# Kernel tuning notes

Hardware: AMD Instinct MI355X
Metric: run time of the kernel (lower is better)

Reference implementation:

```python
import jax, jax.numpy as jnp
import numpy as np

NUM_TOKENS = 2048
HIDDEN = 1024
INTER = 2048
NUM_EXPERTS = 8
TOPK = 2


def setup_inputs() -> dict:
    key = jax.random.key(0)
    k1, k2, k3, k4 = jax.random.split(key, 4)
    hidden_states = jax.random.normal(k1, (NUM_TOKENS, HIDDEN), dtype=jnp.float32)
    router_logits = jax.random.normal(k2, (NUM_TOKENS, NUM_EXPERTS), dtype=jnp.float32)
    # fc1: [E, hidden, 2*intermediate] (proj/gate for SwiGLU), fc2: [E, intermediate, hidden]
    w1 = jax.random.normal(k3, (NUM_EXPERTS, HIDDEN, 2 * INTER), dtype=jnp.float32) * 0.02
    w2 = jax.random.normal(k4, (NUM_EXPERTS, INTER, HIDDEN), dtype=jnp.float32) * 0.02
    return {"hidden_states": hidden_states, "router_logits": router_logits, "w1": w1, "w2": w2}


def _grouped_gemm(x, w, expert_ids):
    """x: [T, D], w: [E, D, O], expert_ids: [T] -> [T, O].
    Tokens are routed to expert expert_ids[t]; equivalent to the sequential
    per-expert GEMM on contiguously sorted tokens. Small fixed loop over E."""
    out = jnp.zeros((x.shape[0], w.shape[-1]), dtype=x.dtype)
    for e in range(w.shape[0]):
        mask = (expert_ids == e)[:, None]
        out = out + jnp.where(mask, x, 0.0) @ w[e]
    return out


def reference(hidden_states, router_logits, w1, w2):
    # top-k routing + softmax over the selected logits
    top_logits, top_idx = jax.lax.top_k(router_logits, TOPK)      # [N, K]
    scores = jax.nn.softmax(top_logits, axis=-1)                  # [N, K]

    flat_idx = top_idx.reshape(-1)                                # [N*K]
    sorted_indices = jnp.argsort(flat_idx)                        # permute tokens grouped by expert
    permuted = hidden_states[sorted_indices // TOPK]              # [N*K, D]
    sorted_experts = flat_idx[sorted_indices]                     # [N*K] expert id per permuted row

    fc1_out = _grouped_gemm(permuted, w1, sorted_experts)         # [N*K, 2*I]
    proj, gate = jnp.split(fc1_out, 2, axis=-1)
    act = jax.nn.silu(proj) * gate                                # SwiGLU
    expert_out = _grouped_gemm(act, w2, sorted_experts)           # [N*K, D]

    # unpermute (scatter back) and weighted combine over top-k
    unpermuted = jnp.zeros_like(expert_out).at[sorted_indices].set(expert_out)
    unpermuted = unpermuted.reshape(-1, TOPK, expert_out.shape[-1])
    return (unpermuted * scores[..., None]).sum(axis=1)           # [N, D]
```

## Files before the change

### kernel.cpp

```cpp
#include <hip/hip_runtime.h>
#include <hip/hip_bf16.h>

constexpr int T = 2048;
constexpr int H = 1024;
constexpr int I = 2048;
constexpr int N2 = 2 * I;
constexpr int RCAP = 5120;
constexpr int MAXT = 40;

constexpr int WS_COUNTS = 0, WS_FILL = 8, WS_OFF = 16, WS_TEXP = 32, WS_TEND = 96;
constexpr int WS_TOPKE = 160, WS_TOPKP = 4256, WS_ROWTOK = 8352, WS_ROWSC = 13472;
constexpr size_t WSB_ZROW = 114688;
constexpr size_t WSB_HSB  = 131072;
constexpr size_t WSB_ACT  = 8u << 20;
constexpr size_t WSB_PW1  = 32u << 20;
constexpr size_t WSB_PW2  = 96u << 20;

constexpr int FC1_BLKS = 32 * MAXT;
constexpr int PW2_BLKS = 4096;
constexpr int PW1_BLKS = 8192;
constexpr int HSB_BLKS = T * H / 2048;

typedef __attribute__((ext_vector_type(4))) float f32x4;
typedef __attribute__((ext_vector_type(8))) short s16x8;

__device__ __forceinline__ short f2bf(float f) {
    unsigned u = __float_as_uint(f);
    u += 0x7FFFu + ((u >> 16) & 1u);
    return (short)(u >> 16);
}

#define MFMA16(a, b, c) __builtin_amdgcn_mfma_f32_16x16x32_bf16(a, b, c, 0, 0, 0)

__device__ __forceinline__ void gl2lds16(const void* g, void* l) {
    __builtin_amdgcn_global_load_lds(
        (const __attribute__((address_space(1))) void*)g,
        (__attribute__((address_space(3))) void*)l, 16, 0, 0);
}

__global__ void router_kernel(const float* __restrict__ logits, int* __restrict__ wsi,
                              float* __restrict__ wsf) {
    int tok = blockIdx.x * 256 + threadIdx.x;
    if (tok >= T) return;
    const float* l = logits + tok * 8;
    float v0 = -1e30f; int i0 = 0;
    #pragma unroll
    for (int i = 0; i < 8; i++) { float v = l[i]; if (v > v0) { v0 = v; i0 = i; } }
    float v1 = -1e30f; int i1 = 0;
    #pragma unroll
    for (int i = 0; i < 8; i++) { if (i == i0) continue; float v = l[i]; if (v > v1) { v1 = v; i1 = i; } }
    float ex = __expf(v1 - v0);
    float inv = 1.f / (1.f + ex);
    wsi[WS_TOPKE + tok * 2] = i0; wsi[WS_TOPKE + tok * 2 + 1] = i1;
    wsf[WS_TOPKP + tok * 2] = inv; wsf[WS_TOPKP + tok * 2 + 1] = ex * inv;
    atomicAdd(&wsi[WS_COUNTS + i0], 1);
    atomicAdd(&wsi[WS_COUNTS + i1], 1);
}

__global__ void plan_kernel(int* __restrict__ wsi) {
    __shared__ int soff[9];
    int t = threadIdx.x;
    if (t == 0) {
        int acc = 0;
        for (int e = 0; e < 8; e++) { soff[e] = acc; acc += (wsi[WS_COUNTS + e] + 127) & ~127; }
        soff[8] = acc;
        for (int e = 0; e < 9; e++) wsi[WS_OFF + e] = soff[e];
    }
    __syncthreads();
    for (int tt = t; tt < MAXT; tt += 256) {
        int rb = tt * 128, ex = -1, en = 0;
        if (rb < soff[8]) {
            for (int e = 0; e < 8; e++)
                if (rb >= soff[e] && rb < soff[e + 1]) { ex = e; en = soff[e] + wsi[WS_COUNTS + e]; }
        }
        wsi[WS_TEXP + tt] = ex; wsi[WS_TEND + tt] = en;
    }
    float* wsf = (float*)wsi;
    for (int r = t; r < RCAP; r += 256) { wsi[WS_ROWTOK + r] = -1; wsf[WS_ROWSC + r] = 0.f; }
    unsigned short* zr = (unsigned short*)((char*)wsi + WSB_ZROW);
    for (int i = t; i < H; i += 256) zr[i] = 0;
}

__global__ void scatter_kernel(int* __restrict__ wsi, float* __restrict__ wsf) {
    int tok = blockIdx.x * 256 + threadIdx.x;
    if (tok >= T) return;
    #pragma unroll
    for (int k = 0; k < 2; k++) {
        int e = wsi[WS_TOPKE + tok * 2 + k];
        float p = wsf[WS_TOPKP + tok * 2 + k];
        int slot = atomicAdd(&wsi[WS_FILL + e], 1);
        int r = wsi[WS_OFF + e] + slot;
        wsi[WS_ROWTOK + r] = tok;
        wsf[WS_ROWSC + r] = p;
    }
}

__global__ __launch_bounds__(256) void prep_kernel(
    const float* __restrict__ w1, unsigned short* __restrict__ pw1,
    const float* __restrict__ hs, unsigned short* __restrict__ hsb) {
    const int t = threadIdx.x;
    if (blockIdx.x < PW1_BLKS) {
        int b = blockIdx.x;
        int k0i = b & 31, ct = (b >> 5) & 31, e = b >> 10;
        const float* src = w1 + (size_t)e * H * N2;
        unsigned short* dst = pw1 + (size_t)b * 4096;
        #pragma unroll
        for (int j = 0; j < 2; j++) {
            int g = t + j * 256;
            int kg = g >> 7, n = g & 127;
            int sub = n >> 5, within = n & 31;
            int col = ((sub & 1) ? I : 0) + ct * 64 + (sub >> 1) * 32 + within;
            int kbase = k0i * 32 + kg * 8;
            const float* sp = src + (size_t)kbase * N2 + col;
            s16x8 s;
            #pragma unroll
            for (int kk = 0; kk < 8; kk++) s[kk] = f2bf(sp[(size_t)kk * N2]);
            *(s16x8*)(dst + g * 8) = s;
        }
    } else {
        int i = ((blockIdx.x - PW1_BLKS) * 256 + t) * 8;
        f32x4 a = *(const f32x4*)(hs + i);
        f32x4 b = *(const f32x4*)(hs + i + 4);
        s16x8 s = {f2bf(a[0]), f2bf(a[1]), f2bf(a[2]), f2bf(a[3]),
                   f2bf(b[0]), f2bf(b[1]), f2bf(b[2]), f2bf(b[3])};
        *(s16x8*)(hsb + i) = s;
    }
}

__global__ __launch_bounds__(256, 2) void fc1_packw2_kernel(
    const unsigned short* __restrict__ hsb, const unsigned short* __restrict__ pw1,
    const int* __restrict__ wsi, const unsigned short* __restrict__ zrow,
    unsigned short* __restrict__ act,
    const float* __restrict__ w2, unsigned short* __restrict__ pw2) {
    __shared__ __align__(16) unsigned short Al[512 * 8];
    __shared__ __align__(16) unsigned short Bl[512 * 8];
    const int t = threadIdx.x;

    if (blockIdx.x >= FC1_BLKS) {
        int b = blockIdx.x - FC1_BLKS;
        int k0i = b & 63, ht = (b >> 6) & 7, e = b >> 9;
        const float* src = w2 + (size_t)e * I * H;
        unsigned short* dst = pw2 + (size_t)b * 4096;
        #pragma unroll
        for (int j = 0; j < 2; j++) {
            int g = t + j * 256;
            int kg = g >> 7, n = g & 127;
            int col = ht * 128 + n;
            int kbase = k0i * 32 + kg * 8;
            const float* sp = src + (size_t)kbase * H + col;
            s16x8 s;
            #pragma unroll
            for (int kk = 0; kk < 8; kk++) s[kk] = f2bf(sp[(size_t)kk * H]);
            *(s16x8*)(dst + g * 8) = s;
        }
        return;
    }

    const int ct = blockIdx.x & 31, rt = blockIdx.x >> 5;
    const int rowb = rt * 128;
    if (rowb >= wsi[WS_OFF + 8]) return;
    const int e = wsi[WS_TEXP + rt];
    const unsigned short* pb = pw1 + (size_t)((e * 32 + ct) * 32) * 4096;

    const int m = t & 127;
    const int tok = wsi[WS_ROWTOK + rowb + m];
    const unsigned short* rp = (tok >= 0) ? (hsb + (size_t)tok * H) : zrow;
    const int kga = t >> 7;

    const int lane = t & 63, w = t >> 6, wr = w >> 1, wc = w & 1;
    const int q = lane >> 4, l16 = lane & 15;

    f32x4 zero = {0.f, 0.f, 0.f, 0.f};
    f32x4 acc[4][4];
    #pragma unroll
    for (int mi = 0; mi < 4; mi++)
        #pragma unroll
        for (int ni = 0; ni < 4; ni++) acc[mi][ni] = zero;

    for (int k0i = 0; k0i < 32; k0i++) {
        const int k0 = k0i * 32;
        gl2lds16(rp + k0 + kga * 8, &Al[t * 8]);
        gl2lds16(rp + k0 + (kga + 2) * 8, &Al[(t + 256) * 8]);
        const unsigned short* ps = pb + (size_t)k0i * 4096;
        gl2lds16(ps + t * 8, &Bl[t * 8]);
        gl2lds16(ps + (t + 256) * 8, &Bl[(t + 256) * 8]);
        __syncthreads();

        s16x8 af[4], bf[4];
        #pragma unroll
        for (int mi = 0; mi < 4; mi++)
            af[mi] = *(const s16x8*)&Al[(q * 128 + wr * 64 + mi * 16 + l16) * 8];
        #pragma unroll
        for (int ni = 0; ni < 4; ni++)
            bf[ni] = *(const s16x8*)&Bl[(q * 128 + wc * 64 + ni * 16 + l16) * 8];
        #pragma unroll
        for (int mi = 0; mi < 4; mi++)
            #pragma unroll
            for (int ni = 0; ni < 4; ni++)
                acc[mi][ni] = MFMA16(af[mi], bf[ni], acc[mi][ni]);
        __syncthreads();
    }

    #pragma unroll
    for (int mi = 0; mi < 4; mi++)
        #pragma unroll
        for (int r = 0; r < 4; r++) {
            int row = rowb + wr * 64 + mi * 16 + q * 4 + r;
            #pragma unroll
            for (int ni = 0; ni < 2; ni++) {
                int col = ct * 64 + wc * 32 + ni * 16 + l16;
                float p = acc[mi][ni][r], g = acc[mi][ni + 2][r];
                float val = p * g / (1.f + __expf(-p));
                act[(size_t)row * I + col] = (unsigned short)f2bf(val);
            }
        }
}

__global__ __launch_bounds__(256, 2) void fc2_kernel(
    const unsigned short* __restrict__ act, const unsigned short* __restrict__ pw2,
    const int* __restrict__ wsi, const float* __restrict__ wsf,
    float* __restrict__ out) {
    __shared__ __align__(16) unsigned short Al[512 * 8];
    __shared__ __align__(16) unsigned short Bl[512 * 8];
    const int t = threadIdx.x;
    const int ht = blockIdx.x, rt = blockIdx.y, ks = blockIdx.z;
    const int rowb = rt * 128;
    if (rowb >= wsi[WS_OFF + 8]) return;
    const int e = wsi[WS_TEXP + rt];
    const unsigned short* pb = pw2 + (size_t)((e * 8 + ht) * 64) * 4096;

    const int m = t & 127;
    const unsigned short* rp = act + (size_t)(rowb + m) * I;
    const int kga = t >> 7;

    const int lane = t & 63, w = t >> 6, wr = w >> 1, wc = w & 1;
    const int q = lane >> 4, l16 = lane & 15;

    f32x4 zero = {0.f, 0.f, 0.f, 0.f};
    f32x4 acc[4][4];
    #pragma unroll
    for (int mi = 0; mi < 4; mi++)
        #pragma unroll
        for (int ni = 0; ni < 4; ni++) acc[mi][ni] = zero;

    for (int k0i = ks * 32; k0i < ks * 32 + 32; k0i++) {
        const int k0 = k0i * 32;
        gl2lds16(rp + k0 + kga * 8, &Al[t * 8]);
        gl2lds16(rp + k0 + (kga + 2) * 8, &Al[(t + 256) * 8]);
        const unsigned short* ps = pb + (size_t)k0i * 4096;
        gl2lds16(ps + t * 8, &Bl[t * 8]);
        gl2lds16(ps + (t + 256) * 8, &Bl[(t + 256) * 8]);
        __syncthreads();

        s16x8 af[4], bf[4];
        #pragma unroll
        for (int mi = 0; mi < 4; mi++)
            af[mi] = *(const s16x8*)&Al[(q * 128 + wr * 64 + mi * 16 + l16) * 8];
        #pragma unroll
        for (int ni = 0; ni < 4; ni++)
            bf[ni] = *(const s16x8*)&Bl[(q * 128 + wc * 64 + ni * 16 + l16) * 8];
        #pragma unroll
        for (int mi = 0; mi < 4; mi++)
            #pragma unroll
            for (int ni = 0; ni < 4; ni++)
                acc[mi][ni] = MFMA16(af[mi], bf[ni], acc[mi][ni]);
        __syncthreads();
    }

    #pragma unroll
    for (int mi = 0; mi < 4; mi++)
        #pragma unroll
        for (int r = 0; r < 4; r++) {
            int row = rowb + wr * 64 + mi * 16 + q * 4 + r;
            int tok = wsi[WS_ROWTOK + row];
            if (tok < 0) continue;
            float sc = wsf[WS_ROWSC + row];
            #pragma unroll
            for (int ni = 0; ni < 4; ni++) {
                int col = ht * 128 + wc * 64 + ni * 16 + l16;
                atomicAdd(&out[(size_t)tok * H + col], acc[mi][ni][r] * sc);
            }
        }
}

extern "C" void kernel_launch(void* const* d_in, const int* in_sizes, int n_in,
                              void* d_out, int out_size, void* d_ws, size_t ws_size,
                              hipStream_t stream) {
    const float* hs     = (const float*)d_in[0];
    const float* logits = (const float*)d_in[1];
    const float* w1     = (const float*)d_in[2];
    const float* w2     = (const float*)d_in[3];
    float* out = (float*)d_out;
    int* wsi = (int*)d_ws;
    float* wsf = (float*)d_ws;
    unsigned short* zrow = (unsigned short*)((char*)d_ws + WSB_ZROW);
    unsigned short* hsb  = (unsigned short*)((char*)d_ws + WSB_HSB);
    unsigned short* act  = (unsigned short*)((char*)d_ws + WSB_ACT);
    unsigned short* pw1  = (unsigned short*)((char*)d_ws + WSB_PW1);
    unsigned short* pw2  = (unsigned short*)((char*)d_ws + WSB_PW2);

    hipMemsetAsync(d_ws, 0, 128, stream);
    hipMemsetAsync(d_out, 0, (size_t)out_size * sizeof(float), stream);

    router_kernel<<<(T + 255) / 256, 256, 0, stream>>>(logits, wsi, wsf);
    plan_kernel<<<1, 256, 0, stream>>>(wsi);
    scatter_kernel<<<(T + 255) / 256, 256, 0, stream>>>(wsi, wsf);
    prep_kernel<<<PW1_BLKS + HSB_BLKS, 256, 0, stream>>>(w1, pw1, hs, hsb);
    fc1_packw2_kernel<<<FC1_BLKS + PW2_BLKS, 256, 0, stream>>>(hsb, pw1, wsi, zrow, act, w2, pw2);
    fc2_kernel<<<dim3(8, MAXT, 2), 256, 0, stream>>>(act, pw2, wsi, wsf, out);
}
```

Baseline: 418.3 us.

## Fuse routing into one kernel and replace fc2 atomics with combine pass

Router, plan and scatter are merged into a single-block routing kernel that uses shared-memory counters, which removes two launches and both memsets. The w2 packing moves from the fc1 kernel into the prep kernel. fc2 now writes its split-K partials to a scratch buffer that reuses the pw1 region, and a new combine kernel does the weighted top-k sum. This replaces the float atomicAdds into the output, but adds a launch and extra buffer traffic, and the w2 packing no longer overlaps with the fc1 GEMM.

Measured after the change: 382.3 us. 1.09x faster.

```diff
diff --git a/kernel.cpp b/kernel.cpp
--- a/kernel.cpp
+++ b/kernel.cpp
@@ -8,18 +8,21 @@
 constexpr int RCAP = 5120;
 constexpr int MAXT = 40;
 
-constexpr int WS_COUNTS = 0, WS_FILL = 8, WS_OFF = 16, WS_TEXP = 32, WS_TEND = 96;
-constexpr int WS_TOPKE = 160, WS_TOPKP = 4256, WS_ROWTOK = 8352, WS_ROWSC = 13472;
+constexpr int WS_OFF = 16;
+constexpr int WS_TEXP = 32;
+constexpr int WS_TOPKP = 4256;
+constexpr int WS_ROWTOK = 8352;
+constexpr int WS_TOKROW = 13472;
 constexpr size_t WSB_ZROW = 114688;
 constexpr size_t WSB_HSB  = 131072;
 constexpr size_t WSB_ACT  = 8u << 20;
 constexpr size_t WSB_PW1  = 32u << 20;
 constexpr size_t WSB_PW2  = 96u << 20;
 
+constexpr int PW1_BLKS = 8192;
+constexpr int PW2_BLKS = 4096;
+constexpr int HSB_BLKS = T * H / 2048;
 constexpr int FC1_BLKS = 32 * MAXT;
-constexpr int PW2_BLKS = 4096;
-constexpr int PW1_BLKS = 8192;
-constexpr int HSB_BLKS = T * H / 2048;
 
 typedef __attribute__((ext_vector_type(4))) float f32x4;
 typedef __attribute__((ext_vector_type(8))) short s16x8;
@@ -38,65 +41,68 @@
         (__attribute__((address_space(3))) void*)l, 16, 0, 0);
 }
 
-__global__ void router_kernel(const float* __restrict__ logits, int* __restrict__ wsi,
-                              float* __restrict__ wsf) {
-    int tok = blockIdx.x * 256 + threadIdx.x;
-    if (tok >= T) return;
-    const float* l = logits + tok * 8;
-    float v0 = -1e30f; int i0 = 0;
-    #pragma unroll
-    for (int i = 0; i < 8; i++) { float v = l[i]; if (v > v0) { v0 = v; i0 = i; } }
-    float v1 = -1e30f; int i1 = 0;
-    #pragma unroll
-    for (int i = 0; i < 8; i++) { if (i == i0) continue; float v = l[i]; if (v > v1) { v1 = v; i1 = i; } }
-    float ex = __expf(v1 - v0);
-    float inv = 1.f / (1.f + ex);
-    wsi[WS_TOPKE + tok * 2] = i0; wsi[WS_TOPKE + tok * 2 + 1] = i1;
-    wsf[WS_TOPKP + tok * 2] = inv; wsf[WS_TOPKP + tok * 2 + 1] = ex * inv;
-    atomicAdd(&wsi[WS_COUNTS + i0], 1);
-    atomicAdd(&wsi[WS_COUNTS + i1], 1);
-}
-
-__global__ void plan_kernel(int* __restrict__ wsi) {
-    __shared__ int soff[9];
-    int t = threadIdx.x;
+__global__ __launch_bounds__(256) void routing_kernel(const float* __restrict__ logits,
+                                                      int* __restrict__ wsi,
+                                                      float* __restrict__ wsf) {
+    __shared__ int cnt[8], base[9], fill[8];
+    const int t = threadIdx.x;
+    if (t < 8) { cnt[t] = 0; fill[t] = 0; }
+    for (int r = t; r < RCAP; r += 256) wsi[WS_ROWTOK + r] = -1;
+    unsigned short* zr = (unsigned short*)((char*)wsi + WSB_ZROW);
+    for (int i = t; i < H; i += 256) zr[i] = 0;
+    __syncthreads();
+
+    int e0a[8], e1a[8];
+    #pragma unroll
+    for (int j = 0; j < 8; j++) {
+        int tok = t * 8 + j;
+        const float* l = logits + tok * 8;
+        float v0 = -1e30f; int i0 = 0;
+        #pragma unroll
+        for (int i = 0; i < 8; i++) { float v = l[i]; if (v > v0) { v0 = v; i0 = i; } }
+        float v1 = -1e30f; int i1 = 0;
+        #pragma unroll
+        for (int i = 0; i < 8; i++) { if (i == i0) continue; float v = l[i]; if (v > v1) { v1 = v; i1 = i; } }
+        float ex = __expf(v1 - v0);
+        float inv = 1.f / (1.f + ex);
+        wsf[WS_TOPKP + tok * 2] = inv;
+        wsf[WS_TOPKP + tok * 2 + 1] = ex * inv;
+        e0a[j] = i0; e1a[j] = i1;
+        atomicAdd(&cnt[i0], 1);
+        atomicAdd(&cnt[i1], 1);
+    }
+    __syncthreads();
     if (t == 0) {
         int acc = 0;
-        for (int e = 0; e < 8; e++) { soff[e] = acc; acc += (wsi[WS_COUNTS + e] + 127) & ~127; }
-        soff[8] = acc;
-        for (int e = 0; e < 9; e++) wsi[WS_OFF + e] = soff[e];
+        for (int e = 0; e < 8; e++) { base[e] = acc; acc += (cnt[e] + 127) & ~127; }
+        base[8] = acc;
+        for (int e = 0; e < 9; e++) wsi[WS_OFF + e] = base[e];
     }
     __syncthreads();
     for (int tt = t; tt < MAXT; tt += 256) {
-        int rb = tt * 128, ex = -1, en = 0;
-        if (rb < soff[8]) {
-            for (int e = 0; e < 8; e++)
-                if (rb >= soff[e] && rb < soff[e + 1]) { ex = e; en = soff[e] + wsi[WS_COUNTS + e]; }
-        }
-        wsi[WS_TEXP + tt] = ex; wsi[WS_TEND + tt] = en;
-    }
-    float* wsf = (float*)wsi;
-    for (int r = t; r < RCAP; r += 256) { wsi[WS_ROWTOK + r] = -1; wsf[WS_ROWSC + r] = 0.f; }
-    unsigned short* zr = (unsigned short*)((char*)wsi + WSB_ZROW);
-    for (int i = t; i < H; i += 256) zr[i] = 0;
-}
-
-__global__ void scatter_kernel(int* __restrict__ wsi, float* __restrict__ wsf) {
-    int tok = blockIdx.x * 256 + threadIdx.x;
-    if (tok >= T) return;
-    #pragma unroll
-    for (int k = 0; k < 2; k++) {
-        int e = wsi[WS_TOPKE + tok * 2 + k];
-        float p = wsf[WS_TOPKP + tok * 2 + k];
-        int slot = atomicAdd(&wsi[WS_FILL + e], 1);
-        int r = wsi[WS_OFF + e] + slot;
-        wsi[WS_ROWTOK + r] = tok;
-        wsf[WS_ROWSC + r] = p;
+        int rb = tt * 128, ex = 0;
+        for (int e = 0; e < 8; e++)
+            if (rb >= base[e] && rb < base[e + 1]) ex = e;
+        wsi[WS_TEXP + tt] = ex;
+    }
+    #pragma unroll
+    for (int j = 0; j < 8; j++) {
+        int tok = t * 8 + j;
+        int ee[2] = {e0a[j], e1a[j]};
+        #pragma unroll
+        for (int k = 0; k < 2; k++) {
+            int e = ee[k];
+            int slot = atomicAdd(&fill[e], 1);
+            int r = base[e] + slot;
+            wsi[WS_ROWTOK + r] = tok;
+            wsi[WS_TOKROW + tok * 2 + k] = r;
+        }
     }
 }
 
 __global__ __launch_bounds__(256) void prep_kernel(
     const float* __restrict__ w1, unsigned short* __restrict__ pw1,
+    const float* __restrict__ w2, unsigned short* __restrict__ pw2,
     const float* __restrict__ hs, unsigned short* __restrict__ hsb) {
     const int t = threadIdx.x;
     if (blockIdx.x < PW1_BLKS) {
@@ -117,27 +123,8 @@
             for (int kk = 0; kk < 8; kk++) s[kk] = f2bf(sp[(size_t)kk * N2]);
             *(s16x8*)(dst + g * 8) = s;
         }
-    } else {
-        int i = ((blockIdx.x - PW1_BLKS) * 256 + t) * 8;
-        f32x4 a = *(const f32x4*)(hs + i);
-        f32x4 b = *(const f32x4*)(hs + i + 4);
-        s16x8 s = {f2bf(a[0]), f2bf(a[1]), f2bf(a[2]), f2bf(a[3]),
-                   f2bf(b[0]), f2bf(b[1]), f2bf(b[2]), f2bf(b[3])};
-        *(s16x8*)(hsb + i) = s;
-    }
-}
-
-__global__ __launch_bounds__(256, 2) void fc1_packw2_kernel(
-    const unsigned short* __restrict__ hsb, const unsigned short* __restrict__ pw1,
-    const int* __restrict__ wsi, const unsigned short* __restrict__ zrow,
-    unsigned short* __restrict__ act,
-    const float* __restrict__ w2, unsigned short* __restrict__ pw2) {
-    __shared__ __align__(16) unsigned short Al[512 * 8];
-    __shared__ __align__(16) unsigned short Bl[512 * 8];
-    const int t = threadIdx.x;
-
-    if (blockIdx.x >= FC1_BLKS) {
-        int b = blockIdx.x - FC1_BLKS;
+    } else if (blockIdx.x < PW1_BLKS + PW2_BLKS) {
+        int b = blockIdx.x - PW1_BLKS;
         int k0i = b & 63, ht = (b >> 6) & 7, e = b >> 9;
         const float* src = w2 + (size_t)e * I * H;
         unsigned short* dst = pw2 + (size_t)b * 4096;
@@ -153,9 +140,23 @@
             for (int kk = 0; kk < 8; kk++) s[kk] = f2bf(sp[(size_t)kk * H]);
             *(s16x8*)(dst + g * 8) = s;
         }
-        return;
-    }
-
+    } else {
+        int i = ((blockIdx.x - PW1_BLKS - PW2_BLKS) * 256 + t) * 8;
+        f32x4 a = *(const f32x4*)(hs + i);
+        f32x4 b = *(const f32x4*)(hs + i + 4);
+        s16x8 s = {f2bf(a[0]), f2bf(a[1]), f2bf(a[2]), f2bf(a[3]),
+                   f2bf(b[0]), f2bf(b[1]), f2bf(b[2]), f2bf(b[3])};
+        *(s16x8*)(hsb + i) = s;
+    }
+}
+
+__global__ __launch_bounds__(256, 2) void fc1_kernel(
+    const unsigned short* __restrict__ hsb, const unsigned short* __restrict__ pw1,
+    const int* __restrict__ wsi, const unsigned short* __restrict__ zrow,
+    unsigned short* __restrict__ act) {
+    __shared__ __align__(16) unsigned short Al[512 * 8];
+    __shared__ __align__(16) unsigned short Bl[512 * 8];
+    const int t = threadIdx.x;
     const int ct = blockIdx.x & 31, rt = blockIdx.x >> 5;
     const int rowb = rt * 128;
     if (rowb >= wsi[WS_OFF + 8]) return;
@@ -218,8 +219,7 @@
 
 __global__ __launch_bounds__(256, 2) void fc2_kernel(
     const unsigned short* __restrict__ act, const unsigned short* __restrict__ pw2,
-    const int* __restrict__ wsi, const float* __restrict__ wsf,
-    float* __restrict__ out) {
+    const int* __restrict__ wsi, float* __restrict__ eo) {
     __shared__ __align__(16) unsigned short Al[512 * 8];
     __shared__ __align__(16) unsigned short Bl[512 * 8];
     const int t = threadIdx.x;
@@ -267,20 +267,37 @@
         __syncthreads();
     }
 
+    float* ed = eo + (size_t)ks * RCAP * H;
     #pragma unroll
     for (int mi = 0; mi < 4; mi++)
         #pragma unroll
         for (int r = 0; r < 4; r++) {
             int row = rowb + wr * 64 + mi * 16 + q * 4 + r;
-            int tok = wsi[WS_ROWTOK + row];
-            if (tok < 0) continue;
-            float sc = wsf[WS_ROWSC + row];
             #pragma unroll
             for (int ni = 0; ni < 4; ni++) {
                 int col = ht * 128 + wc * 64 + ni * 16 + l16;
-                atomicAdd(&out[(size_t)tok * H + col], acc[mi][ni][r] * sc);
+                ed[(size_t)row * H + col] = acc[mi][ni][r];
             }
         }
+}
+
+__global__ __launch_bounds__(256) void combine_kernel(
+    const float* __restrict__ eo, const int* __restrict__ wsi,
+    const float* __restrict__ wsf, float* __restrict__ out) {
+    const int tok = blockIdx.x;
+    const int r0 = wsi[WS_TOKROW + tok * 2], r1 = wsi[WS_TOKROW + tok * 2 + 1];
+    const float s0 = wsf[WS_TOPKP + tok * 2], s1 = wsf[WS_TOPKP + tok * 2 + 1];
+    const float* a0 = eo + (size_t)r0 * H;
+    const float* a1 = eo + (size_t)RCAP * H + (size_t)r0 * H;
+    const float* b0 = eo + (size_t)r1 * H;
+    const float* b1 = eo + (size_t)RCAP * H + (size_t)r1 * H;
+    const int c = threadIdx.x * 4;
+    f32x4 va0 = *(const f32x4*)(a0 + c), va1 = *(const f32x4*)(a1 + c);
+    f32x4 vb0 = *(const f32x4*)(b0 + c), vb1 = *(const f32x4*)(b1 + c);
+    f32x4 r;
+    #pragma unroll
+    for (int i = 0; i < 4; i++) r[i] = s0 * (va0[i] + va1[i]) + s1 * (vb0[i] + vb1[i]);
+    *(f32x4*)(out + (size_t)tok * H + c) = r;
 }
 
 extern "C" void kernel_launch(void* const* d_in, const int* in_sizes, int n_in,
@@ -298,14 +315,11 @@
     unsigned short* act  = (unsigned short*)((char*)d_ws + WSB_ACT);
     unsigned short* pw1  = (unsigned short*)((char*)d_ws + WSB_PW1);
     unsigned short* pw2  = (unsigned short*)((char*)d_ws + WSB_PW2);
-
-    hipMemsetAsync(d_ws, 0, 128, stream);
-    hipMemsetAsync(d_out, 0, (size_t)out_size * sizeof(float), stream);
-
-    router_kernel<<<(T + 255) / 256, 256, 0, stream>>>(logits, wsi, wsf);
-    plan_kernel<<<1, 256, 0, stream>>>(wsi);
-    scatter_kernel<<<(T + 255) / 256, 256, 0, stream>>>(wsi, wsf);
-    prep_kernel<<<PW1_BLKS + HSB_BLKS, 256, 0, stream>>>(w1, pw1, hs, hsb);
-    fc1_packw2_kernel<<<FC1_BLKS + PW2_BLKS, 256, 0, stream>>>(hsb, pw1, wsi, zrow, act, w2, pw2);
-    fc2_kernel<<<dim3(8, MAXT, 2), 256, 0, stream>>>(act, pw2, wsi, wsf, out);
-}
+    float* eo = (float*)((char*)d_ws + WSB_PW1);
+
+    routing_kernel<<<1, 256, 0, stream>>>(logits, wsi, wsf);
+    prep_kernel<<<PW1_BLKS + PW2_BLKS + HSB_BLKS, 256, 0, stream>>>(w1, pw1, w2, pw2, hs, hsb);
+    fc1_kernel<<<FC1_BLKS, 256, 0, stream>>>(hsb, pw1, wsi, zrow, act);
+    fc2_kernel<<<dim3(8, MAXT, 2), 256, 0, stream>>>(act, pw2, wsi, eo);
+    combine_kernel<<<T, 256, 0, stream>>>(eo, wsi, wsf, out);
+}
```
